# Kernel optimization log

Measured on AMD Instinct MI355X. Metric: run time of the kernel, lower is better.

Reference implementation:

```python
import jax, jax.numpy as jnp
import numpy as np

B, S, E, H, WIN = 16, 4096, 512, 8, 64


def setup_inputs() -> dict:
    key = jax.random.key(0)
    k1, k2, k3 = jax.random.split(key, 3)
    bound = 1.0 / np.sqrt(E)
    x = jax.random.normal(k1, (B, S, E), dtype=jnp.float32)
    # nn.MultiheadAttention params: packed in-projection (3E, E) + bias, out-projection (E, E) + bias
    W_in = jax.random.uniform(k2, (3 * E, E), minval=-bound, maxval=bound, dtype=jnp.float32)
    b_in = jnp.zeros((3 * E,), dtype=jnp.float32)
    W_out = jax.random.uniform(k3, (E, E), minval=-bound, maxval=bound, dtype=jnp.float32)
    b_out = jnp.zeros((E,), dtype=jnp.float32)
    return {"x": x, "W_in": W_in, "b_in": b_in, "W_out": W_out, "b_out": b_out}


def reference(x, W_in, b_in, W_out, b_out):
    # Faithful to the torch module: nn.MultiheadAttention has batch_first=False,
    # over the batch axis, with window positions acting as the MHA batch.
    Bb, Ss, Ee = x.shape
    Dh = Ee // H
    nW = Ss // WIN
    xp = x.reshape(Bb, nW, WIN, Ee).transpose(1, 2, 0, 3)
    qkv = xp @ W_in.T + b_in
    q, k, v = jnp.split(qkv, 3, axis=-1)
    q = q.reshape(nW, WIN, Bb, H, Dh)
    k = k.reshape(nW, WIN, Bb, H, Dh)
    v = v.reshape(nW, WIN, Bb, H, Dh)
    scale = 1.0 / np.sqrt(Dh)
    scores = jnp.einsum('nwahd,nwbhd->nwhab', q, k) * scale
    attn = jax.nn.softmax(scores, axis=-1)
    o = jnp.einsum('nwhab,nwbhd->nwahd', attn, v).reshape(nW, WIN, Bb, Ee)
    out = o @ W_out.T + b_out
    return out.transpose(2, 0, 1, 3).reshape(Bb, Ss, Ee)
```

## Files before the change

### kernel.cpp

```cpp
#include <hip/hip_runtime.h>


#define S_LEN  4096
#define E_DIM  512
#define QKV_LD 1536

typedef __bf16 bf16x8 __attribute__((ext_vector_type(8)));
typedef __bf16 bf16x4 __attribute__((ext_vector_type(4)));
typedef short  s16x4  __attribute__((ext_vector_type(4)));
typedef float  f32x4  __attribute__((ext_vector_type(4)));

__device__ __forceinline__ float b2f(unsigned int u16) {
    return __uint_as_float(u16 << 16);
}
__device__ __forceinline__ unsigned short f2bf(float f) {
    unsigned int u = __float_as_uint(f);
    u += 0x7fffu + ((u >> 16) & 1u);
    return (unsigned short)(u >> 16);
}
__device__ __forceinline__ void unpack8(uint4 u, float* f) {
    f[0] = b2f(u.x & 0xffffu); f[1] = b2f(u.x >> 16);
    f[2] = b2f(u.y & 0xffffu); f[3] = b2f(u.y >> 16);
    f[4] = b2f(u.z & 0xffffu); f[5] = b2f(u.z >> 16);
    f[6] = b2f(u.w & 0xffffu); f[7] = b2f(u.w >> 16);
}
__device__ __forceinline__ uint4 pack8(const float* f) {
    uint4 u;
    u.x = (unsigned)f2bf(f[0]) | ((unsigned)f2bf(f[1]) << 16);
    u.y = (unsigned)f2bf(f[2]) | ((unsigned)f2bf(f[3]) << 16);
    u.z = (unsigned)f2bf(f[4]) | ((unsigned)f2bf(f[5]) << 16);
    u.w = (unsigned)f2bf(f[6]) | ((unsigned)f2bf(f[7]) << 16);
    return u;
}

__device__ __forceinline__ bool detect_f32(const unsigned int* __restrict__ probe) {
    unsigned int w = probe[threadIdx.x & 63];
    unsigned int e = (w >> 23) & 0xffu;
    unsigned long long b = __ballot(e >= 90u && e <= 160u);
    return __popcll(b) >= 32;
}

__device__ __forceinline__ void gload16(const unsigned short* g, unsigned short* l) {
    __builtin_amdgcn_global_load_lds(
        (const __attribute__((address_space(1))) unsigned int*)g,
        (__attribute__((address_space(3))) unsigned int*)l, 16, 0, 0);
}

template<int N>
__device__ __forceinline__ void waitvm() {
    asm volatile("s_waitcnt vmcnt(%0)" :: "n"(N) : "memory");
}

__device__ __forceinline__ f32x4 mfma16bf(s16x4 a, s16x4 b, f32x4 c) {
    f32x4 d;
    asm volatile("s_nop 3\n\t"
                 "v_mfma_f32_16x16x16_bf16 %0, %1, %2, %3\n\t"
                 "s_nop 7\n\t"
                 "s_nop 7"
                 : "=v"(d) : "v"(a), "v"(b), "v"(c));
    return d;
}

template<bool F32>
__device__ __forceinline__ uint4 cvt8(const void* src, long off) {
    if (F32) {
        const float* p = (const float*)src + off;
        float4 a = *(const float4*)p, b = *(const float4*)(p + 4);
        float f[8] = {a.x, a.y, a.z, a.w, b.x, b.y, b.z, b.w};
        return pack8(f);
    }
    return *(const uint4*)((const unsigned short*)src + off);
}

template<bool F32>
__device__ void conv_w_body(const void* Win, const void* Wout, const void* bin,
                            const void* bout, unsigned short* dst)
{
    int c = blockIdx.x * 256 + threadIdx.x;
    if (c >= 131328) return;
    const void* src; long soff; long doff = (long)c * 8;
    if (c < 98304)       { src = Win;  soff = doff; }
    else if (c < 131072) { src = Wout; soff = doff - 786432; }
    else if (c < 131264) { src = bin;  soff = doff - 1048576; }
    else                 { src = bout; soff = doff - 1050112; }
    *(uint4*)(dst + doff) = cvt8<F32>(src, soff);
}
__global__ __launch_bounds__(256) void conv_w_k(const void* Win, const void* Wout,
        const void* bin, const void* bout, unsigned short* dst,
        const unsigned int* __restrict__ probe)
{
    if (detect_f32(probe)) conv_w_body<true>(Win, Wout, bin, bout, dst);
    else                   conv_w_body<false>(Win, Wout, bin, bout, dst);
}

template<bool F32>
__device__ void conv_x_body(const void* __restrict__ x, unsigned short* __restrict__ xb,
                            int s0, int lgC)
{
    long c = (long)blockIdx.x * 256 + threadIdx.x;
    const long row = c >> 6;
    const int  col = (int)(c & 63) * 8;
    const long srcRow = (row >> lgC) * S_LEN + s0 + (row & ((1L << lgC) - 1));
    *(uint4*)(xb + row * E_DIM + col) = cvt8<F32>(x, srcRow * E_DIM + col);
}
__global__ __launch_bounds__(256) void conv_x_k(const void* __restrict__ x,
        unsigned short* __restrict__ xb, int s0, int lgC,
        const unsigned int* __restrict__ probe)
{
    if (detect_f32(probe)) conv_x_body<true>(x, xb, s0, lgC);
    else                   conv_x_body<false>(x, xb, s0, lgC);
}

template<int BM, int BN, int WM, int WN, int MODE>
__device__ void gemm8_body(const unsigned short* __restrict__ A,
                           const unsigned short* __restrict__ W,
                           const unsigned short* __restrict__ bias,
                           void* __restrict__ C, int s0, int lgC, int nbx,
                           bool f32out)
{
    constexpr int BK   = 32;
    constexpr int MF   = BM / WM / 16;
    constexpr int NF   = BN / WN / 16;
    constexpr int NL   = (BM + BN) * BK / 256 / 16;
    constexpr int TILE = (BM + BN) * BK;
    constexpr int NT   = E_DIM / BK;
    constexpr int PF   = 3;
    constexpr int lda  = (MODE == 1) ? E_DIM : QKV_LD;

    __shared__ __align__(16) unsigned short Ls[4 * TILE];

    const int nwg = gridDim.x;
    const int id0 = blockIdx.x;
    const int id  = (id0 & 7) * (nwg >> 3) + (id0 >> 3);
    const int nby = nwg / nbx;
    const int by  = id % nby;
    const int bx  = id / nby;

    const int tid  = threadIdx.x;
    const int wave = tid >> 6;
    const int lane = tid & 63;
    const int wm   = wave / WN;
    const int wn   = wave % WN;
    const int lrow = lane & 15;
    const int lq   = lane >> 4;
    const long m0  = (long)bx * BM;
    const int  n0  = by * BN;

    const unsigned short* src[NL];
    unsigned short*       dst[NL];
    #pragma unroll
    for (int j = 0; j < NL; ++j) {
        const int Lg  = wave * NL + j;
        const int row = Lg * 16 + (lane >> 2);
        const int ls  = (lane & 3) ^ ((row >> 1) & 3);
        src[j] = (row < BM) ? A + (m0 + row) * lda + ls * 8
                            : W + (long)(n0 + row - BM) * E_DIM + ls * 8;
        dst[j] = Ls + Lg * 512;
    }

    f32x4 acc[MF][NF];
    #pragma unroll
    for (int i = 0; i < MF; ++i)
        #pragma unroll
        for (int j = 0; j < NF; ++j)
            acc[i][j] = (f32x4){0.f, 0.f, 0.f, 0.f};

    #pragma unroll
    for (int t = 0; t < PF; ++t)
        #pragma unroll
        for (int j = 0; j < NL; ++j)
            gload16(src[j] + t * BK, dst[j] + t * TILE);

    #pragma unroll
    for (int it = 0; it < NT; ++it) {
        __builtin_amdgcn_s_barrier();
        asm volatile("" ::: "memory");
        if (it + PF < NT) {
            #pragma unroll
            for (int j = 0; j < NL; ++j)
                gload16(src[j] + (it + PF) * BK, dst[j] + ((it + PF) & 3) * TILE);
            waitvm<PF * NL>();
        } else if (NT - 1 - it == 2) {
            waitvm<2 * NL>();
        } else if (NT - 1 - it == 1) {
            waitvm<NL>();
        } else {
            waitvm<0>();
        }
        __builtin_amdgcn_sched_barrier(0);
        __builtin_amdgcn_s_barrier();
        asm volatile("" ::: "memory");

        const unsigned short* Ab = Ls + (it & 3) * TILE;
        const unsigned short* Bb = Ab + BM * BK;
        bf16x8 bfr[NF];
        #pragma unroll
        for (int ni = 0; ni < NF; ++ni) {
            const int r = wn * (BN / WN) + ni * 16 + lrow;
            bfr[ni] = *(const bf16x8*)(Bb + r * 32 + ((lq ^ ((r >> 1) & 3)) << 3));
        }
        #pragma unroll
        for (int mh = 0; mh < MF; mh += 4) {
            bf16x8 afr[4];
            #pragma unroll
            for (int u = 0; u < 4; ++u) {
                const int r = wm * (BM / WM) + (mh + u) * 16 + lrow;
                afr[u] = *(const bf16x8*)(Ab + r * 32 + ((lq ^ ((r >> 1) & 3)) << 3));
            }
            __builtin_amdgcn_s_setprio(1);
            #pragma unroll
            for (int u = 0; u < 4; ++u)
                #pragma unroll
                for (int ni = 0; ni < NF; ++ni)
                    acc[mh + u][ni] = __builtin_amdgcn_mfma_f32_16x16x32_bf16(
                        afr[u], bfr[ni], acc[mh + u][ni], 0, 0, 0);
            __builtin_amdgcn_s_setprio(0);
        }
        __builtin_amdgcn_sched_barrier(0);
    }

    #pragma unroll
    for (int mi = 0; mi < MF; ++mi)
        #pragma unroll
        for (int ni = 0; ni < NF; ++ni) {
            const int col = n0 + wn * (BN / WN) + ni * 16 + lrow;
            const float bv = b2f(bias[col]);
            #pragma unroll
            for (int r = 0; r < 4; ++r) {
                const long row = m0 + wm * (BM / WM) + mi * 16 + lq * 4 + r;
                const float v = acc[mi][ni][r] + bv;
                if (MODE == 1) {
                    ((unsigned short*)C)[row * QKV_LD + col] = f2bf(v);
                } else {
                    const long g = ((row >> lgC) * S_LEN + s0 + (row & ((1L << lgC) - 1)))
                                   * E_DIM + col;
                    if (f32out) ((float*)C)[g] = v;
                    else        ((unsigned short*)C)[g] = f2bf(v);
                }
            }
        }
}

__global__ __launch_bounds__(512, 2) void gemm1_k(const unsigned short* __restrict__ A,
        const unsigned short* __restrict__ W, const unsigned short* __restrict__ bias,
        unsigned short* __restrict__ C, int nbx)
{
    gemm8_body<256, 256, 2, 4, 1>(A, W, bias, C, 0, 0, nbx, false);
}

__global__ __launch_bounds__(512, 2) void gemm2_k(const unsigned short* __restrict__ A,
        const unsigned short* __restrict__ W, const unsigned short* __restrict__ bias,
        void* __restrict__ C, int s0, int lgC, int nbx,
        const unsigned int* __restrict__ probe)
{
    const bool f32out = detect_f32(probe);
    gemm8_body<256, 128, 4, 2, 2>(A, W, bias, C, s0, lgC, nbx, f32out);
}

__global__ __launch_bounds__(256) void attn_kernel(unsigned short* __restrict__ qkv,
                                                   int Cs)
{
    const int wave = threadIdx.x >> 6;
    const int lane = threadIdx.x & 63;
    const int task = blockIdx.x * 4 + wave;
    const int h    = task & 7;
    const int sc   = task >> 3;
    const int a    = lane & 15;
    const int g    = lane >> 4;

    const unsigned short* qbase =
        qkv + ((long)a * Cs + sc) * QKV_LD + h * 64 + g * 8;
    const bf16x8 qf0 = *(const bf16x8*)(qbase);
    const bf16x8 qf1 = *(const bf16x8*)(qbase + 32);
    const bf16x8 kf0 = *(const bf16x8*)(qbase + 512);
    const bf16x8 kf1 = *(const bf16x8*)(qbase + 544);

    unsigned short vv[4][4];
    const unsigned short* vbase = qkv + (long)sc * QKV_LD + 1024 + h * 64 + a;
    #pragma unroll
    for (int j = 0; j < 4; ++j) {
        const unsigned short* vr = vbase + (long)(g * 4 + j) * Cs * QKV_LD;
        #pragma unroll
        for (int t = 0; t < 4; ++t) vv[t][j] = vr[t * 16];
    }

    f32x4 s = (f32x4){0.f, 0.f, 0.f, 0.f};
    s = __builtin_amdgcn_mfma_f32_16x16x32_bf16(kf0, qf0, s, 0, 0, 0);
    s = __builtin_amdgcn_mfma_f32_16x16x32_bf16(kf1, qf1, s, 0, 0, 0);

    float m = fmaxf(fmaxf(s[0], s[1]), fmaxf(s[2], s[3]));
    m = fmaxf(m, __shfl_xor(m, 16));
    m = fmaxf(m, __shfl_xor(m, 32));
    float p[4], sum = 0.f;
    #pragma unroll
    for (int r = 0; r < 4; ++r) { p[r] = __expf((s[r] - m) * 0.125f); sum += p[r]; }
    sum += __shfl_xor(sum, 16);
    sum += __shfl_xor(sum, 32);
    const float inv = 1.f / sum;

    bf16x4 phi, plo;
    #pragma unroll
    for (int r = 0; r < 4; ++r) {
        const float pn = p[r] * inv;
        const __bf16 hi = (__bf16)pn;
        phi[r] = hi;
        plo[r] = (__bf16)(pn - (float)hi);
    }
    const s16x4 phs = __builtin_bit_cast(s16x4, phi);
    const s16x4 pls = __builtin_bit_cast(s16x4, plo);

    unsigned short* obase = qkv + ((long)a * Cs + sc) * QKV_LD + h * 64 + g * 4;
    const f32x4 zero = (f32x4){0.f, 0.f, 0.f, 0.f};
    #pragma unroll
    for (int t = 0; t < 4; ++t) {
        s16x4 vf;
        #pragma unroll
        for (int j = 0; j < 4; ++j) vf[j] = (short)vv[t][j];
        f32x4 o = mfma16bf(vf, phs, zero);
        o = mfma16bf(vf, pls, o);
        uint2 st;
        st.x = (unsigned)f2bf(o[0]) | ((unsigned)f2bf(o[1]) << 16);
        st.y = (unsigned)f2bf(o[2]) | ((unsigned)f2bf(o[3]) << 16);
        *(uint2*)(obase + t * 16) = st;
    }
}

extern "C" void kernel_launch(void* const* d_in, const int* in_sizes, int n_in,
                              void* d_out, int out_size, void* d_ws, size_t ws_size,
                              hipStream_t stream)
{
    const void* x     = d_in[0];
    const void* W_in  = d_in[1];
    const void* b_in  = d_in[2];
    const void* W_out = d_in[3];
    const void* b_out = d_in[4];
    const unsigned int* probe = (const unsigned int*)d_in[0];

    const bool big = ws_size >= 270536704ull;
    const int  Cs  = big ? S_LEN : 1024;
    const int  lgC = big ? 12 : 10;
    const int  nch = big ? 1 : 4;
    const long M   = 16L * Cs;
    const int  nbx = (int)(M / 256);

    unsigned short* qkv = (unsigned short*)d_ws;
    unsigned short* xb  = qkv + (size_t)M * QKV_LD;
    unsigned short* wb  = xb + (size_t)M * E_DIM;
    const unsigned short* Wi = wb;
    const unsigned short* Wo = wb + 786432;
    const unsigned short* bi = wb + 1048576;
    const unsigned short* bo = wb + 1050112;

    hipLaunchKernelGGL(conv_w_k, dim3(514), dim3(256), 0, stream,
                       W_in, W_out, b_in, b_out, wb, probe);

    for (int c = 0; c < nch; ++c) {
        const int s0 = c * Cs;
        hipLaunchKernelGGL(conv_x_k, dim3((int)(M / 4)), dim3(256), 0, stream,
                           x, xb, s0, lgC, probe);
        hipLaunchKernelGGL(gemm1_k, dim3(nbx * 6), dim3(512), 0, stream,
                           xb, Wi, bi, qkv, nbx);
        hipLaunchKernelGGL(attn_kernel, dim3(Cs * 2), dim3(256), 0, stream, qkv, Cs);
        hipLaunchKernelGGL(gemm2_k, dim3(nbx * 4), dim3(512), 0, stream,
                           qkv, Wo, bo, d_out, s0, lgC, nbx, probe);
    }
}
```

Measured before the change: 480.5 us.

## Interleave GEMM main loop into two half-phases with split global prefetch

Restructures the GEMM K-loop so that each iteration splits the A-fragment LDS reads, the global prefetch loads and the MFMA work into two halves separated by barriers. The aim is to overlap global-to-LDS traffic with matrix-core work and to move the vmcnt wait to the end of the iteration instead of the start. It adds extra barriers per iteration and depends on the wait-count bookkeeping being correct for the 4-stage ring buffer.

```diff
diff --git a/kernel.cpp b/kernel.cpp
--- a/kernel.cpp
+++ b/kernel.cpp
@@ -121,7 +121,9 @@
     constexpr int BK   = 32;
     constexpr int MF   = BM / WM / 16;
     constexpr int NF   = BN / WN / 16;
-    constexpr int NL   = (BM + BN) * BK / 256 / 16;
+    constexpr int MH   = MF / 2;
+    constexpr int NL   = (BM + BN) * BK / 4096;
+    constexpr int NLa  = (NL + 1) / 2;
     constexpr int TILE = (BM + BN) * BK;
     constexpr int NT   = E_DIM / BK;
     constexpr int PF   = 3;
@@ -170,53 +172,71 @@
         #pragma unroll
         for (int j = 0; j < NL; ++j)
             gload16(src[j] + t * BK, dst[j] + t * TILE);
+    waitvm<2 * NL>();
+    __builtin_amdgcn_s_barrier();
+    asm volatile("" ::: "memory");
 
     #pragma unroll
     for (int it = 0; it < NT; ++it) {
-        __builtin_amdgcn_s_barrier();
-        asm volatile("" ::: "memory");
-        if (it + PF < NT) {
-            #pragma unroll
-            for (int j = 0; j < NL; ++j)
-                gload16(src[j] + (it + PF) * BK, dst[j] + ((it + PF) & 3) * TILE);
-            waitvm<PF * NL>();
-        } else if (NT - 1 - it == 2) {
-            waitvm<2 * NL>();
-        } else if (NT - 1 - it == 1) {
-            waitvm<NL>();
-        } else {
-            waitvm<0>();
-        }
-        __builtin_amdgcn_sched_barrier(0);
-        __builtin_amdgcn_s_barrier();
-        asm volatile("" ::: "memory");
-
         const unsigned short* Ab = Ls + (it & 3) * TILE;
         const unsigned short* Bb = Ab + BM * BK;
-        bf16x8 bfr[NF];
+
+        bf16x8 bfr[NF], af1[MH];
         #pragma unroll
         for (int ni = 0; ni < NF; ++ni) {
             const int r = wn * (BN / WN) + ni * 16 + lrow;
             bfr[ni] = *(const bf16x8*)(Bb + r * 32 + ((lq ^ ((r >> 1) & 3)) << 3));
         }
         #pragma unroll
-        for (int mh = 0; mh < MF; mh += 4) {
-            bf16x8 afr[4];
-            #pragma unroll
-            for (int u = 0; u < 4; ++u) {
-                const int r = wm * (BM / WM) + (mh + u) * 16 + lrow;
-                afr[u] = *(const bf16x8*)(Ab + r * 32 + ((lq ^ ((r >> 1) & 3)) << 3));
-            }
-            __builtin_amdgcn_s_setprio(1);
-            #pragma unroll
-            for (int u = 0; u < 4; ++u)
-                #pragma unroll
-                for (int ni = 0; ni < NF; ++ni)
-                    acc[mh + u][ni] = __builtin_amdgcn_mfma_f32_16x16x32_bf16(
-                        afr[u], bfr[ni], acc[mh + u][ni], 0, 0, 0);
-            __builtin_amdgcn_s_setprio(0);
-        }
+        for (int u = 0; u < MH; ++u) {
+            const int r = wm * (BM / WM) + u * 16 + lrow;
+            af1[u] = *(const bf16x8*)(Ab + r * 32 + ((lq ^ ((r >> 1) & 3)) << 3));
+        }
+        if (it + PF < NT) {
+            #pragma unroll
+            for (int j = 0; j < NLa; ++j)
+                gload16(src[j] + (it + PF) * BK, dst[j] + ((it + PF) & 3) * TILE);
+        }
+        __builtin_amdgcn_s_barrier();
         __builtin_amdgcn_sched_barrier(0);
+        __builtin_amdgcn_s_setprio(1);
+        #pragma unroll
+        for (int u = 0; u < MH; ++u)
+            #pragma unroll
+            for (int ni = 0; ni < NF; ++ni)
+                acc[u][ni] = __builtin_amdgcn_mfma_f32_16x16x32_bf16(
+                    af1[u], bfr[ni], acc[u][ni], 0, 0, 0);
+        __builtin_amdgcn_s_setprio(0);
+        __builtin_amdgcn_sched_barrier(0);
+        __builtin_amdgcn_s_barrier();
+
+        bf16x8 af2[MF - MH];
+        #pragma unroll
+        for (int u = 0; u < MF - MH; ++u) {
+            const int r = wm * (BM / WM) + (MH + u) * 16 + lrow;
+            af2[u] = *(const bf16x8*)(Ab + r * 32 + ((lq ^ ((r >> 1) & 3)) << 3));
+        }
+        if (it + PF < NT) {
+            #pragma unroll
+            for (int j = NLa; j < NL; ++j)
+                gload16(src[j] + (it + PF) * BK, dst[j] + ((it + PF) & 3) * TILE);
+        }
+        __builtin_amdgcn_s_barrier();
+        __builtin_amdgcn_sched_barrier(0);
+        __builtin_amdgcn_s_setprio(1);
+        #pragma unroll
+        for (int u = 0; u < MF - MH; ++u)
+            #pragma unroll
+            for (int ni = 0; ni < NF; ++ni)
+                acc[MH + u][ni] = __builtin_amdgcn_mfma_f32_16x16x32_bf16(
+                    af2[u], bfr[ni], acc[MH + u][ni], 0, 0, 0);
+        __builtin_amdgcn_s_setprio(0);
+        __builtin_amdgcn_sched_barrier(0);
+        if (it + PF < NT)           waitvm<2 * NL>();
+        else if (it == NT - 3)      waitvm<NL>();
+        else if (it == NT - 2)      waitvm<0>();
+        __builtin_amdgcn_s_barrier();
+        asm volatile("" ::: "memory");
     }
 
     #pragma unroll
```

After: 492.2 us. +2.4%, slower.
